# Performance work log

Hardware: AMD Instinct MI355X
Metric: run time of the kernel (lower is better)

The kernel has to match this reference:

```python
import jax, jax.numpy as jnp
import numpy as np


def _pairwise_dist(a, b):
    # Euclidean distances between [B,N,3] and [B,M,3] -> [B,N,M], matching torch.cdist(p=2)
    sq = (jnp.sum(a * a, axis=-1)[:, :, None]
          + jnp.sum(b * b, axis=-1)[:, None, :]
          - 2.0 * jnp.einsum('bnd,bmd->bnm', a, b))
    return jnp.sqrt(jnp.maximum(sq, 0.0))


def setup_inputs() -> dict:
    key = jax.random.key(0)
    k1, k2 = jax.random.split(key)
    xyz1 = jax.random.normal(k1, (4, 8192, 3), dtype=jnp.float32)
    xyz2 = jax.random.normal(k2, (4, 8192, 3), dtype=jnp.float32)
    return {"xyz1": xyz1, "xyz2": xyz2}


def reference(xyz1, xyz2):
    d = _pairwise_dist(xyz1, xyz2)          # [B,N,M]
    dist1 = jnp.min(d, axis=2)              # [B,N] nearest in xyz2 for each xyz1 point
    idx1 = jnp.argmin(d, axis=2).astype(jnp.int32)
    dist2 = jnp.min(d, axis=1)              # [B,M] nearest in xyz1 for each xyz2 point
    idx2 = jnp.argmin(d, axis=1).astype(jnp.int32)
    return (dist1, dist2, idx1, idx2)
```

## Files before the change

kernel.cpp:

```cpp
#include <hip/hip_runtime.h>
#include <math.h>


#define BATCH 4
#define NPTS  8192
#define NQ    65536
#define SPLIT 16
#define CHUNK 512
#define MARGIN 2e-4f

typedef float f2 __attribute__((ext_vector_type(2)));

__global__ __launch_bounds__(256)
void prep_k(const float* __restrict__ xyz1, const float* __restrict__ xyz2,
            float4* __restrict__ pk) {
#pragma clang fp contract(off)
    int tid = blockIdx.x * blockDim.x + threadIdx.x;
    int src = tid >> 14;
    int b   = (tid >> 12) & 3;
    int p   = tid & 4095;
    const float* sp = (src == 0 ? xyz1 : xyz2) + ((size_t)b * NPTS + 2 * p) * 3;
    float x0 = sp[0], y0 = sp[1], z0 = sp[2];
    float x1 = sp[3], y1 = sp[4], z1 = sp[5];
    float t0 = __fadd_rn(__fadd_rn(__fmul_rn(x0, x0), __fmul_rn(y0, y0)), __fmul_rn(z0, z0));
    float t1 = __fadd_rn(__fadd_rn(__fmul_rn(x1, x1), __fmul_rn(y1, y1)), __fmul_rn(z1, z1));
    size_t base = (size_t)(src * 4 + b) * 8192;
    pk[base + 2 * p + 0] = make_float4(x0, x1, y0, y1);
    pk[base + 2 * p + 1] = make_float4(z0, z1, t0, t1);
}

__global__ __launch_bounds__(256)
void phaseA(const float* __restrict__ xyz1, const float* __restrict__ xyz2,
            const float4* __restrict__ pk, float* __restrict__ qsA) {
#pragma clang fp contract(fast)
    int bid = blockIdx.x;
    int sg  = bid & 3;
    int qw  = (bid >> 2) & 127;
    int b   = (bid >> 9) & 3;
    int dir = bid >> 11;

    int t    = threadIdx.x;
    int lane = t & 63;
    int w    = t >> 6;
    int s    = __builtin_amdgcn_readfirstlane(sg * 4 + w);

    int q = qw * 64 + lane;
    const float* qp = (dir == 0 ? xyz1 : xyz2) + ((size_t)b * NPTS + q) * 3;
    float qx = qp[0], qy = qp[1], qz = qp[2];
    float qq = __fadd_rn(__fadd_rn(__fmul_rn(qx, qx), __fmul_rn(qy, qy)),
                         __fmul_rn(qz, qz));
    float n2x = -(qx + qx), n2y = -(qy + qy), n2z = -(qz + qz);
    f2 NX = {n2x, n2x}, NY = {n2y, n2y}, NZ = {n2z, n2z};

    int tslot = (dir == 0 ? 4 : 0) + b;
    const float4* tp = pk + (size_t)tslot * 8192 + (size_t)s * 512;

    float m0 = INFINITY, m1 = INFINITY, m2 = INFINITY, m3 = INFINITY;

    #define PQS(A, B, M)                                                    \
    {                                                                       \
        f2 X = {A.x, A.y}, Y = {A.z, A.w}, Z = {B.x, B.y}, T = {B.z, B.w};  \
        f2 r = ((T + NZ * Z) + NY * Y) + NX * X;                            \
        M = fminf(fminf(r.x, r.y), M);                                      \
    }

    #pragma unroll 2
    for (int g = 0; g < 64; ++g) {
        float4 A0 = tp[8 * g + 0], B0 = tp[8 * g + 1];
        float4 A1 = tp[8 * g + 2], B1 = tp[8 * g + 3];
        float4 A2 = tp[8 * g + 4], B2 = tp[8 * g + 5];
        float4 A3 = tp[8 * g + 6], B3 = tp[8 * g + 7];
        PQS(A0, B0, m0) PQS(A1, B1, m1) PQS(A2, B2, m2) PQS(A3, B3, m3)
    }
    #undef PQS

    float r = fminf(fminf(m0, m1), fminf(m2, m3));
    int qidx = (dir * BATCH + b) * NPTS + q;
    qsA[(size_t)qidx * SPLIT + s] = qq + r;
}

__global__ __launch_bounds__(256)
void mergeA(const float* __restrict__ qsA, unsigned* __restrict__ maskq) {
    int tid = blockIdx.x * blockDim.x + threadIdx.x;
    float ms[SPLIT];
    float m = INFINITY;
    #pragma unroll
    for (int s = 0; s < SPLIT; ++s) {
        ms[s] = qsA[(size_t)tid * SPLIT + s];
        m = fminf(m, ms[s]);
    }
    float thr = m + MARGIN;
    unsigned mask = 0;
    #pragma unroll
    for (int s = 0; s < SPLIT; ++s)
        if (ms[s] <= thr) mask |= (1u << s);
    maskq[tid] = mask;
}

__global__ __launch_bounds__(256)
void phaseB(const float* __restrict__ xyz1, const float* __restrict__ xyz2,
            const float4* __restrict__ pk, const unsigned* __restrict__ maskq,
            float* __restrict__ out) {
#pragma clang fp contract(off)
    int t    = threadIdx.x;
    int w    = t >> 6;
    int lane = t & 63;
    int qidx = blockIdx.x * 4 + w;
    int dir  = qidx >> 15;
    int rem  = qidx & 32767;
    int b    = rem >> 13;
    int q    = rem & (NPTS - 1);

    const float* qp = (dir == 0 ? xyz1 : xyz2) + ((size_t)b * NPTS + q) * 3;
    float qx = qp[0], qy = qp[1], qz = qp[2];
    float qq = __fadd_rn(__fadd_rn(__fmul_rn(qx, qx), __fmul_rn(qy, qy)),
                         __fmul_rn(qz, qz));
    float q2x = qx + qx, q2y = qy + qy, q2z = qz + qz;

    int tslot = (dir == 0 ? 4 : 0) + b;
    const float4* tb = pk + (size_t)tslot * 8192;

    unsigned mask = maskq[qidx];
    float bdl = INFINITY;
    int ff = 0, ll = 0;

    while (mask) {
        int s = __builtin_ctz(mask);
        mask &= mask - 1;
        const float4* tp = tb + (size_t)s * 512;
        int jb = s * CHUNK;
        #pragma unroll
        for (int i = 0; i < 4; ++i) {
            int pi = i * 64 + lane;
            float4 A = tp[2 * pi + 0];
            float4 B = tp[2 * pi + 1];
            {
                float u1 = __fmul_rn(q2z, B.x);
                float u2 = __fmul_rn(q2y, A.z);
                float a1 = __fadd_rn(u1, u2);
                float u3 = __fmul_rn(q2x, A.x);
                float e2 = __fadd_rn(a1, u3);
                float ss = __fadd_rn(qq, B.z);
                float qs = __fsub_rn(ss, e2);
                float d  = sqrtf(fmaxf(qs, 0.0f));
                int j = jb + 2 * pi;
                bool lt = d < bdl, le = d <= bdl;
                ff = lt ? j : ff; ll = le ? j : ll; bdl = fminf(bdl, d);
            }
            {
                float u1 = __fmul_rn(q2z, B.y);
                float u2 = __fmul_rn(q2y, A.w);
                float a1 = __fadd_rn(u1, u2);
                float u3 = __fmul_rn(q2x, A.y);
                float e2 = __fadd_rn(a1, u3);
                float ss = __fadd_rn(qq, B.w);
                float qs = __fsub_rn(ss, e2);
                float d  = sqrtf(fmaxf(qs, 0.0f));
                int j = jb + 2 * pi + 1;
                bool lt = d < bdl, le = d <= bdl;
                ff = lt ? j : ff; ll = le ? j : ll; bdl = fminf(bdl, d);
            }
        }
    }

    #pragma unroll
    for (int m = 1; m < 64; m <<= 1) {
        float ob = __shfl_xor(bdl, m);
        int   of = __shfl_xor(ff, m);
        int   ol = __shfl_xor(ll, m);
        bool lt = ob < bdl, eq = ob == bdl;
        ff = lt ? of : (eq ? min(ff, of) : ff);
        ll = lt ? ol : (eq ? max(ll, ol) : ll);
        bdl = fminf(bdl, ob);
    }

    if (lane == 0) {
        int span = ll - ff;
        int idx  = (span > 1200) ? ll : ff;
        const size_t SEG = (size_t)BATCH * NPTS;
        out[(size_t)dir * SEG + rem]           = bdl;
        out[2 * SEG + (size_t)dir * SEG + rem] = (float)idx;
    }
}

extern "C" void kernel_launch(void* const* d_in, const int* in_sizes, int n_in,
                              void* d_out, int out_size, void* d_ws, size_t ws_size,
                              hipStream_t stream) {
    const float* xyz1 = (const float*)d_in[0];
    const float* xyz2 = (const float*)d_in[1];
    float* out = (float*)d_out;

    char* wsp = (char*)d_ws;
    float4*   pk    = (float4*)(wsp);
    float*    qsA   = (float*)(wsp + (1u << 20));
    unsigned* maskq = (unsigned*)(wsp + (5u << 20));

    prep_k<<<128, 256, 0, stream>>>(xyz1, xyz2, pk);
    phaseA<<<4096, 256, 0, stream>>>(xyz1, xyz2, pk, qsA);
    mergeA<<<NQ / 256, 256, 0, stream>>>(qsA, maskq);
    phaseB<<<NQ / 4, 256, 0, stream>>>(xyz1, xyz2, pk, maskq, out);
}
```

Baseline: 106.4 us.

## Fuse split-merge into phaseB and remap phaseA blocks to one chunk per block

Drops the separate mergeA kernel. phaseB now reads the 16 per-split partial minima with one wave, reduces them with shuffles and builds the candidate mask with a ballot. phaseA is reorganised so each block covers 256 queries against a single chunk instead of 64 queries against four chunks, and its unroll factor goes from 2 to 4. This removes one launch and a mask round trip through memory, in exchange for a different chunk-reuse pattern in phaseA and a few extra shuffles in phaseB.

```diff
diff --git a/kernel.cpp b/kernel.cpp
--- a/kernel.cpp
+++ b/kernel.cpp
@@ -34,17 +34,14 @@
             const float4* __restrict__ pk, float* __restrict__ qsA) {
 #pragma clang fp contract(fast)
     int bid = blockIdx.x;
-    int sg  = bid & 3;
-    int qw  = (bid >> 2) & 127;
+    int s   = bid & 15;
+    int qb  = (bid >> 4) & 31;
     int b   = (bid >> 9) & 3;
     int dir = bid >> 11;
 
-    int t    = threadIdx.x;
-    int lane = t & 63;
-    int w    = t >> 6;
-    int s    = __builtin_amdgcn_readfirstlane(sg * 4 + w);
+    int t = threadIdx.x;
+    int q = qb * 256 + t;
 
-    int q = qw * 64 + lane;
     const float* qp = (dir == 0 ? xyz1 : xyz2) + ((size_t)b * NPTS + q) * 3;
     float qx = qp[0], qy = qp[1], qz = qp[2];
     float qq = __fadd_rn(__fadd_rn(__fmul_rn(qx, qx), __fmul_rn(qy, qy)),
@@ -64,7 +61,7 @@
         M = fminf(fminf(r.x, r.y), M);                                      \
     }
 
-    #pragma unroll 2
+    #pragma unroll 4
     for (int g = 0; g < 64; ++g) {
         float4 A0 = tp[8 * g + 0], B0 = tp[8 * g + 1];
         float4 A1 = tp[8 * g + 2], B1 = tp[8 * g + 3];
@@ -80,26 +77,8 @@
 }
 
 __global__ __launch_bounds__(256)
-void mergeA(const float* __restrict__ qsA, unsigned* __restrict__ maskq) {
-    int tid = blockIdx.x * blockDim.x + threadIdx.x;
-    float ms[SPLIT];
-    float m = INFINITY;
-    #pragma unroll
-    for (int s = 0; s < SPLIT; ++s) {
-        ms[s] = qsA[(size_t)tid * SPLIT + s];
-        m = fminf(m, ms[s]);
-    }
-    float thr = m + MARGIN;
-    unsigned mask = 0;
-    #pragma unroll
-    for (int s = 0; s < SPLIT; ++s)
-        if (ms[s] <= thr) mask |= (1u << s);
-    maskq[tid] = mask;
-}
-
-__global__ __launch_bounds__(256)
 void phaseB(const float* __restrict__ xyz1, const float* __restrict__ xyz2,
-            const float4* __restrict__ pk, const unsigned* __restrict__ maskq,
+            const float4* __restrict__ pk, const float* __restrict__ qsA,
             float* __restrict__ out) {
 #pragma clang fp contract(off)
     int t    = threadIdx.x;
@@ -111,6 +90,13 @@
     int b    = rem >> 13;
     int q    = rem & (NPTS - 1);
 
+    float val = (lane < SPLIT) ? qsA[(size_t)qidx * SPLIT + lane] : INFINITY;
+    float m = val;
+    #pragma unroll
+    for (int mm = 1; mm < 64; mm <<= 1) m = fminf(m, __shfl_xor(m, mm));
+    unsigned long long bal = __ballot(lane < SPLIT && val <= m + MARGIN);
+    unsigned mask = (unsigned)(bal & 0xFFFFu);
+
     const float* qp = (dir == 0 ? xyz1 : xyz2) + ((size_t)b * NPTS + q) * 3;
     float qx = qp[0], qy = qp[1], qz = qp[2];
     float qq = __fadd_rn(__fadd_rn(__fmul_rn(qx, qx), __fmul_rn(qy, qy)),
@@ -120,7 +106,6 @@
     int tslot = (dir == 0 ? 4 : 0) + b;
     const float4* tb = pk + (size_t)tslot * 8192;
 
-    unsigned mask = maskq[qidx];
     float bdl = INFINITY;
     int ff = 0, ll = 0;
 
@@ -164,10 +149,10 @@
     }
 
     #pragma unroll
-    for (int m = 1; m < 64; m <<= 1) {
-        float ob = __shfl_xor(bdl, m);
-        int   of = __shfl_xor(ff, m);
-        int   ol = __shfl_xor(ll, m);
+    for (int mm = 1; mm < 64; mm <<= 1) {
+        float ob = __shfl_xor(bdl, mm);
+        int   of = __shfl_xor(ff, mm);
+        int   ol = __shfl_xor(ll, mm);
         bool lt = ob < bdl, eq = ob == bdl;
         ff = lt ? of : (eq ? min(ff, of) : ff);
         ll = lt ? ol : (eq ? max(ll, ol) : ll);
@@ -191,12 +176,10 @@
     float* out = (float*)d_out;
 
     char* wsp = (char*)d_ws;
-    float4*   pk    = (float4*)(wsp);
-    float*    qsA   = (float*)(wsp + (1u << 20));
-    unsigned* maskq = (unsigned*)(wsp + (5u << 20));
+    float4* pk  = (float4*)(wsp);
+    float*  qsA = (float*)(wsp + (1u << 20));
 
     prep_k<<<128, 256, 0, stream>>>(xyz1, xyz2, pk);
     phaseA<<<4096, 256, 0, stream>>>(xyz1, xyz2, pk, qsA);
-    mergeA<<<NQ / 256, 256, 0, stream>>>(qsA, maskq);
-    phaseB<<<NQ / 4, 256, 0, stream>>>(xyz1, xyz2, pk, maskq, out);
+    phaseB<<<NQ / 4, 256, 0, stream>>>(xyz1, xyz2, pk, qsA, out);
 }
```

Result: faster. 98.32 us (-7.6%).
